# Performance work log

Hardware: AMD Instinct MI355X
Metric: run time of the kernel (lower is better)

Reference implementation:

```python
import jax, jax.numpy as jnp
import numpy as np

N, E, G, K, C = 16000, 256000, 64, 10, 32
NB, MH, NP, NE, ND, SH, RH = 8, 16, 4, 3, 6, 9, 64
R_MAX, AVG_NBR, P = 5.0, 16.0, 6
LVALS = jnp.array([0, 1, 1, 1, 2, 2, 2, 2, 2])  # l of each lm slot (l<=2)


def _silu(x):
    return x * jax.nn.sigmoid(x)


def _sph(v):
    # real spherical harmonics up to l=2 on unit vectors, e3nn 'component' normalization
    x, y, z = v[:, 0], v[:, 1], v[:, 2]
    s3, s5, s15 = 3.0 ** 0.5, 5.0 ** 0.5, 15.0 ** 0.5
    return jnp.stack([
        jnp.ones_like(x),
        s3 * x, s3 * y, s3 * z,
        s15 * x * y, s15 * y * z, 0.5 * s5 * (3.0 * z * z - 1.0),
        s15 * x * z, 0.5 * s15 * (x * x - y * y)], axis=-1)


def setup_inputs():
    key = jax.random.key(0)
    ks = jax.random.split(key, 26)

    def w(k, shape):
        fan_in = shape[-2] if len(shape) > 1 else shape[-1]
        return jax.random.normal(k, shape, jnp.float32) / np.float32(np.sqrt(fan_in))

    elems = jax.random.randint(ks[0], (N,), 0, K)
    return {
        'positions': 2.0 * jax.random.normal(ks[1], (N, 3), jnp.float32),
        'node_attrs': jax.nn.one_hot(elems, K, dtype=jnp.float32),
        'shifts': jnp.zeros((E, 3), jnp.float32),
        'E0': jax.random.normal(ks[2], (K,), jnp.float32),
        'W_embed': w(ks[3], (K, C)),
        'W_up': w(ks[4], (2, C, C)),
        'W_r1': w(ks[5], (2, NB, RH)),
        'W_r2': w(ks[6], (2, RH, RH)),
        'W_r3': w(ks[7], (2, RH, SH * C)),
        'W_sc': w(ks[8], (2, K, 3, C, C)),
        'W_prod': w(ks[9], (2, 3, C, C)),
        'Wc': w(ks[10], (2, 3, K, C, C)),
        'We1': w(ks[11], (2, C, MH)),
        'We2': w(ks[12], (2, MH, NE)),
        'Wi1': w(ks[13], (2, C, MH)),
        'Wi2': w(ks[14], (2, MH, NP)),
        'Wdp': w(ks[15], (2, C, ND)),
        'Wd1': w(ks[16], (NP, RH)),
        'bd1': jnp.zeros((RH,), jnp.float32),
        'Wd2': w(ks[17], (RH, NE)),
        'bd2': jnp.zeros((NE,), jnp.float32),
        'edge_index': jax.random.randint(ks[18], (2, E), 0, N).astype(jnp.int32),
        'batch': jnp.sort(jax.random.randint(ks[19], (N,), 0, G)).astype(jnp.int32),
    }


def _forward(edge_index, batch, positions, node_attrs, shifts, E0, W_embed, W_up,
             W_r1, W_r2, W_r3, W_sc, W_prod, Wc, We1, We2, Wi1, Wi2, Wdp,
             Wd1, bd1, Wd2, bd2):
    src, dst = edge_index[0], edge_index[1]
    vec = positions[src] - positions[dst] + shifts          # [E,3]
    r = jnp.sqrt(jnp.sum(vec * vec, axis=-1) + 1e-12)       # [E]
    sh = _sph(vec / r[:, None])                              # [E,9]
    # Bessel radial basis with polynomial cutoff envelope (p=6)
    u = r / R_MAX
    n = jnp.arange(1, NB + 1, dtype=jnp.float32)
    bess = jnp.sqrt(2.0 / R_MAX) * jnp.sin(n * jnp.pi * u[:, None]) / r[:, None]
    env = (1.0 - 0.5 * (P + 1) * (P + 2) * u ** P + P * (P + 2) * u ** (P + 1)
           - 0.5 * P * (P + 1) * u ** (P + 2))
    env = jnp.where(u < 1.0, env, 0.0)
    edge_feats = bess * env[:, None]                         # [E,NB]

    e0 = jax.ops.segment_sum(node_attrs @ E0, batch, num_segments=G)  # [G]
    feats = jnp.zeros((N, SH, C), jnp.float32).at[:, 0, :].set(node_attrs @ W_embed)

    eng_sum = jnp.zeros((G, NE), jnp.float32)
    inv_sum = jnp.zeros((G, NP), jnp.float32)
    dip_sum = jnp.zeros((G, 3, ND), jnp.float32)
    for l in range(2):
        up = feats[:, 0, :] @ W_up[l]                        # [N,C]
        Rw = _silu(edge_feats @ W_r1[l])
        Rw = _silu(Rw @ W_r2[l])
        Rw = (Rw @ W_r3[l]).reshape(E, SH, C)                # per-edge TP weights
        msg = Rw * sh[:, :, None] * up[src][:, None, :]      # [E,9,C]
        agg = jax.ops.segment_sum(msg, dst, num_segments=N) / AVG_NBR
        sc = jnp.einsum('nk,klcd,nlc->nld', node_attrs, W_sc[l][:, LVALS], feats)
        mixed = jnp.einsum('nlc,lcd->nld', agg, W_prod[l][LVALS])
        new = mixed + sc
        s0 = new[:, 0, :]
        # element-dependent symmetric-contraction on invariants (correlation 3)
        corr = (jnp.einsum('nk,kcd,nc->nd', node_attrs, Wc[l, 0], s0)
                + jnp.einsum('nk,kcd,nc->nd', node_attrs, Wc[l, 1], s0 * s0)
                + jnp.einsum('nk,kcd,nc->nd', node_attrs, Wc[l, 2], s0 * s0 * s0))
        feats = new.at[:, 0, :].add(corr)
        s = feats[:, 0, :]
        v = feats[:, 1:4, :]                                  # l=1 block [N,3,C]
        node_E = _silu(s @ We1[l]) @ We2[l]                   # [N,NE]
        node_inv = _silu(s @ Wi1[l]) @ Wi2[l]                 # [N,NP]
        node_dip = jnp.einsum('nvc,cd->nvd', v, Wdp[l])       # [N,3,ND]
        eng_sum = eng_sum + jax.ops.segment_sum(node_E, batch, num_segments=G)
        inv_sum = inv_sum + jax.ops.segment_sum(node_inv, batch, num_segments=G)
        dip_sum = dip_sum + jax.ops.segment_sum(node_dip, batch, num_segments=G)

    decoded = _silu(inv_sum @ Wd1 + bd1) @ Wd2 + bd2 + e0[:, None]   # [G,NE]
    total_e = eng_sum + e0[:, None]                                   # [G,NE]
    dip = jnp.transpose(dip_sum, (0, 2, 1))                           # [G,ND,3]
    return jnp.concatenate([decoded, total_e, dip.reshape(G, 3 * ND)], axis=-1)


def reference(positions, node_attrs, shifts, E0, W_embed, W_up, W_r1, W_r2, W_r3,
              W_sc, W_prod, Wc, We1, We2, Wi1, Wi2, Wdp, Wd1, bd1, Wd2, bd2,
              edge_index, batch):
    return _forward(edge_index, batch, positions, node_attrs, shifts, E0, W_embed,
                    W_up, W_r1, W_r2, W_r3, W_sc, W_prod, Wc, We1, We2, Wi1, Wi2,
                    Wdp, Wd1, bd1, Wd2, bd2)
```

## Files before the change

### kernel.cpp

```cpp
#include <hip/hip_runtime.h>
#include <math.h>

#define NN 16000
#define EE 256000
#define GG 64
#define KK 10
#define CC 32
#define NBB 8
#define MHH 16
#define NPP 4
#define NEE 3
#define NDD 6
#define SHH 9
#define RHH 64
#define SHCC (SHH*CC)

typedef __attribute__((ext_vector_type(8))) short s8b;
typedef __attribute__((ext_vector_type(4))) float f32x4;

__device__ __forceinline__ float siluf(float x){ return x / (1.0f + __expf(-x)); }
__device__ __forceinline__ short bf16rne(float x){
  unsigned u = __float_as_uint(x);
  unsigned r = u + 0x7FFFu + ((u>>16)&1u);
  return (short)(r>>16);
}

__global__ __launch_bounds__(256) void init_kernel(
    const float* __restrict__ attrs, const float* __restrict__ E0v,
    const float* __restrict__ Wemb, const float* __restrict__ Wup0,
    const int* __restrict__ batch,
    int* __restrict__ kidx, float* __restrict__ feats, float* __restrict__ e0g,
    float* __restrict__ up)
{
  int t = blockIdx.x*blockDim.x + threadIdx.x;
  if (t >= NN*CC) return;
  int n = t >> 5, d = t & 31;
  const float* a = attrs + n*KK;
  int k = 0; float best = a[0];
  #pragma unroll
  for (int j=1;j<KK;j++){ float v=a[j]; if (v>best){best=v;k=j;} }
  float* f = feats + n*SHCC;
  f[d] = Wemb[k*CC+d];
  #pragma unroll
  for (int s=1;s<SHH;s++) f[s*CC+d] = 0.0f;
  float accu = 0.0f;
  #pragma unroll
  for (int c=0;c<CC;c++) accu += Wemb[k*CC+c]*Wup0[c*CC+d];
  up[n*CC+d] = accu * 0.0625f;
  if (d==0){ kidx[n]=k; atomicAdd(&e0g[batch[n]], E0v[k]); }
}

__global__ __launch_bounds__(256) void hist_kernel(
    const int* __restrict__ ei, int* __restrict__ rowptr)
{
  int e = blockIdx.x*256 + threadIdx.x;
  if (e < EE) atomicAdd(&rowptr[ei[EE+e]+1], 1);
}

__global__ __launch_bounds__(1024) void scan_kernel(
    int* __restrict__ rowptr, int* __restrict__ cursor)
{
  __shared__ int part[1024];
  const int t = threadIdx.x;
  const int SEG = 16;
  const int base = t*SEG;
  int a[SEG];
  int run = 0;
  #pragma unroll
  for (int i=0;i<SEG;i++){
    int idx = base+i;
    int v = (idx <= NN) ? rowptr[idx] : 0;
    run += v; a[i] = run;
  }
  part[t] = run;
  __syncthreads();
  for (int off=1; off<1024; off<<=1){
    int v = (t>=off) ? part[t-off] : 0;
    __syncthreads();
    part[t] += v;
    __syncthreads();
  }
  int offset = (t>0) ? part[t-1] : 0;
  #pragma unroll
  for (int i=0;i<SEG;i++){
    int idx = base+i;
    if (idx <= NN){
      int val = offset + a[i];
      rowptr[idx] = val;
      if (idx < NN) cursor[idx] = val;
    }
  }
}

__global__ __launch_bounds__(256) void scatter_kernel(
    const int* __restrict__ ei, int* __restrict__ cursor, int* __restrict__ sorted)
{
  int e = blockIdx.x*256 + threadIdx.x;
  if (e < EE){
    int d = ei[EE+e];
    int p = atomicAdd(&cursor[d], 1);
    sorted[p] = e;
  }
}

__global__ __launch_bounds__(256, 2) void edge_kernel(
    const float* __restrict__ pos, const float* __restrict__ shifts,
    const float* __restrict__ Wr1, const float* __restrict__ Wr2,
    const float* __restrict__ Wr3, const float* __restrict__ up,
    const int* __restrict__ ei, const int* __restrict__ sorted,
    float* __restrict__ agg)
{
  __shared__ alignas(16) short sW3T[SHCC*RHH];
  __shared__ alignas(16) short sW2T[RHH*RHH];
  __shared__ alignas(16) float sW1T[RHH*NBB];
  __shared__ alignas(16) char  uni[64*65*4];
  __shared__ alignas(16) float sh_l[4][16*12];
  __shared__ int dst_l[64];

  for (int i=threadIdx.x; i<RHH*SHCC; i+=256){
    int kk = i/SHCC, o = i - kk*SHCC;
    sW3T[(o*RHH + kk) ^ ((o&7)<<3)] = bf16rne(Wr3[i]);
  }
  for (int i=threadIdx.x; i<RHH*RHH; i+=256){
    int k = i>>6, kk = i&63;
    sW2T[(kk*RHH + k) ^ ((kk&7)<<3)] = bf16rne(Wr2[i]);
  }
  for (int i=threadIdx.x; i<NBB*RHH; i+=256){
    int b = i>>6, k = i&63;
    sW1T[k*NBB + b] = Wr1[i];
  }
  __syncthreads();

  const int tid  = threadIdx.x;
  const int lane = tid & 63;
  const int el   = lane & 15;
  const int r    = lane >> 4;
  const int wv   = tid >> 6;
  float* msg = (float*)uni;
  float* efw = (float*)(uni + wv*512);
  short* h2w = (short*)(uni + 2048 + wv*2304);
  float* shw = sh_l[wv];
  const f32x4 zf = {0.f,0.f,0.f,0.f};
  const float PI_ = 3.14159265358979323846f;

  for (int w = blockIdx.x; w < EE/64; w += gridDim.x) {
    const int e0 = w*64 + wv*16;
    {
      const int e = sorted[e0 + el];
      const int src = ei[e], dst = ei[EE+e];
      if (r==0) dst_l[wv*16+el] = dst;
      float x = pos[src*3+0]-pos[dst*3+0]+shifts[e*3+0];
      float y = pos[src*3+1]-pos[dst*3+1]+shifts[e*3+1];
      float z = pos[src*3+2]-pos[dst*3+2]+shifts[e*3+2];
      float rr = sqrtf(x*x+y*y+z*z+1e-12f);
      float ir = 1.0f/rr;
      x*=ir; y*=ir; z*=ir;
      const float S3=1.7320508075688772f, S5h=1.1180339887498949f;
      const float S15=3.872983346207417f, S15h=1.9364916731037085f;
      if (r==0){ shw[el*12+0]=1.0f;            shw[el*12+1]=S3*x;     shw[el*12+2]=S3*y; }
      else if (r==1){ shw[el*12+3]=S3*z;       shw[el*12+4]=S15*x*y;  shw[el*12+5]=S15*y*z; }
      else if (r==2){ shw[el*12+6]=S5h*(3.0f*z*z-1.0f); shw[el*12+7]=S15*x*z; shw[el*12+8]=S15h*(x*x-y*y); }
      float u = rr*0.2f;
      float u2=u*u, u3=u2*u, u6=u3*u3;
      float env = 1.0f - 28.0f*u6 + 48.0f*u6*u - 21.0f*u6*u2;
      env = (u<1.0f)? env : 0.0f;
      env *= ir * 0.6324555320336759f;
      float n1 = (float)(r+1), n2 = (float)(r+5);
      efw[el*8 + r]     = __sinf(n1*PI_*u)*env;
      efw[el*8 + r + 4] = __sinf(n2*PI_*u)*env;
    }
    float h1v[16];
    {
      f32x4 efa = *(const f32x4*)&efw[el*8];
      f32x4 efb = *(const f32x4*)&efw[el*8+4];
      #pragma unroll
      for (int s=0;s<2;s++){
        #pragma unroll
        for (int j=0;j<8;j++){
          int kq = 32*s + 8*r + j;
          f32x4 wa = *(const f32x4*)&sW1T[kq*NBB];
          f32x4 wb = *(const f32x4*)&sW1T[kq*NBB+4];
          float acc = efa[0]*wa[0]+efa[1]*wa[1]+efa[2]*wa[2]+efa[3]*wa[3]
                    + efb[0]*wb[0]+efb[1]*wb[1]+efb[2]*wb[2]+efb[3]*wb[3];
          h1v[s*8+j] = siluf(acc);
        }
      }
    }
    s8b a1s0, a1s1;
    #pragma unroll
    for (int j=0;j<8;j++){ a1s0[j]=bf16rne(h1v[j]); a1s1[j]=bf16rne(h1v[8+j]); }

    f32x4 aw2[4];
    #pragma unroll
    for (int t=0;t<4;t++){
      int kk = 16*t + el;
      int sw = (kk&7)<<3;
      s8b b0 = *(const s8b*)&sW2T[(kk*RHH + 8*r     ) ^ sw];
      s8b b1 = *(const s8b*)&sW2T[(kk*RHH + 8*r + 32) ^ sw];
      f32x4 acc = __builtin_amdgcn_mfma_f32_16x16x32_bf16(a1s0, b0, zf, 0,0,0);
      aw2[t]    = __builtin_amdgcn_mfma_f32_16x16x32_bf16(a1s1, b1, acc, 0,0,0);
    }
    #pragma unroll
    for (int t=0;t<4;t++){
      #pragma unroll
      for (int reg=0;reg<4;reg++)
        h2w[(4*r+reg)*72 + 16*t + el] = bf16rne(siluf(aw2[t][reg]));
    }
    s8b a2s0 = *(const s8b*)&h2w[el*72 + 8*r];
    s8b a2s1 = *(const s8b*)&h2w[el*72 + 32 + 8*r];

    float upv[4][2];
    #pragma unroll
    for (int reg=0;reg<4;reg++){
      int ee = sorted[e0 + 4*r + reg];
      int s_ = ei[ee];
      upv[reg][0] = up[s_*CC + el];
      upv[reg][1] = up[s_*CC + 16 + el];
    }
    __syncthreads();

    unsigned long long runmask;
    {
      bool flag = (lane==0) || (dst_l[lane] != dst_l[lane-1]);
      runmask = __ballot(flag);
    }

    #pragma unroll
    for (int c=0;c<5;c++){
      const int tBeg = 4*c;
      const int tEnd = (c<4)? (tBeg+4) : 18;
      for (int t=tBeg;t<tEnd;t++){
        int o = 16*t + el;
        int sw = (o&7)<<3;
        s8b b0 = *(const s8b*)&sW3T[(o*RHH + 8*r     ) ^ sw];
        s8b b1 = *(const s8b*)&sW3T[(o*RHH + 8*r + 32) ^ sw];
        f32x4 acc = __builtin_amdgcn_mfma_f32_16x16x32_bf16(a2s0, b0, zf, 0,0,0);
        acc       = __builtin_amdgcn_mfma_f32_16x16x32_bf16(a2s1, b1, acc, 0,0,0);
        const int sidx = t>>1, spar = t&1;
        #pragma unroll
        for (int reg=0;reg<4;reg++){
          float v = acc[reg] * shw[(4*r+reg)*12 + sidx] * upv[reg][spar];
          msg[(wv*16 + 4*r + reg)*65 + 16*(t-tBeg) + el] = v;
        }
      }
      __syncthreads();
      {
        const int col = (c<4) ? (tid & 63) : (tid & 31);
        const bool act = (c<4) || ((tid & 63) < 32);
        const int q = tid >> 6;
        const int obase = 64*c;
        if (act){
          unsigned long long m = runmask;
          int j = 0;
          while (m){
            int s = __builtin_ctzll(m);
            m &= (m-1);
            int en = m ? __builtin_ctzll(m) : 64;
            if ((j & 3) == q){
              float a = 0.0f;
              for (int i=s;i<en;i++) a += msg[i*65 + col];
              atomicAdd(agg + (size_t)dst_l[s]*SHCC + obase + col, a);
            }
            j++;
          }
        }
      }
      __syncthreads();
    }
  }
}

__global__ __launch_bounds__(256) void node_kernel(
    const float* __restrict__ feats, float* __restrict__ fout,
    const float* __restrict__ agg,
    const int* __restrict__ kidx, const int* __restrict__ batch,
    const float* __restrict__ Wsc, const float* __restrict__ Wprod,
    const float* __restrict__ WcL,
    const float* __restrict__ We1, const float* __restrict__ We2,
    const float* __restrict__ Wi1, const float* __restrict__ Wi2,
    const float* __restrict__ Wdp, const float* __restrict__ Wup1,
    float* __restrict__ up,
    float* __restrict__ eng, float* __restrict__ inv, float* __restrict__ dip)
{
  __shared__ float s0l[8][CC];
  __shared__ float sul[8][CC];
  __shared__ float vl[8][3][CC];
  __shared__ float hl[8][CC];
  const int t = threadIdx.x;
  const int nn = t >> 5;
  const int d = t & 31;
  const int n = blockIdx.x*8 + nn;
  const int k = kidx[n];
  const int b = batch[n];
  const float* fin = feats + n*SHCC;
  const float* ag = agg + n*SHCC;
  float nw[SHH];
  const int LV[SHH] = {0,1,1,1,2,2,2,2,2};
  #pragma unroll
  for (int s=0;s<SHH;s++){
    const int lv = LV[s];
    const float* wp  = Wprod + lv*CC*CC + d;
    const float* wsc = Wsc + (k*3+lv)*CC*CC + d;
    float acc = 0.0f;
    #pragma unroll
    for (int c=0;c<CC;c++)
      acc += ag[s*CC+c]*wp[c*CC] + fin[s*CC+c]*wsc[c*CC];
    nw[s] = acc;
  }
  s0l[nn][d] = nw[0];
  vl[nn][0][d] = nw[1]; vl[nn][1][d] = nw[2]; vl[nn][2][d] = nw[3];
  __syncthreads();
  float corr = 0.0f;
  {
    const float* wc0 = WcL + (0*KK+k)*CC*CC + d;
    const float* wc1 = WcL + (1*KK+k)*CC*CC + d;
    const float* wc2 = WcL + (2*KK+k)*CC*CC + d;
    #pragma unroll
    for (int c=0;c<CC;c++){
      float s0 = s0l[nn][c];
      float s2 = s0*s0;
      corr += s0*wc0[c*CC] + s2*wc1[c*CC] + s2*s0*wc2[c*CC];
    }
  }
  float su = nw[0] + corr;
  sul[nn][d] = su;
  float* fo = fout + n*SHCC;
  fo[d] = su;
  #pragma unroll
  for (int s=1;s<SHH;s++) fo[s*CC+d] = nw[s];
  __syncthreads();
  {
    const int m = d & 15;
    const float* W = (d < MHH) ? We1 : Wi1;
    float acc = 0.0f;
    #pragma unroll
    for (int c=0;c<CC;c++) acc += sul[nn][c]*W[c*MHH+m];
    hl[nn][d] = siluf(acc);
  }
  {
    float acc = 0.0f;
    #pragma unroll
    for (int c=0;c<CC;c++) acc += sul[nn][c]*Wup1[c*CC+d];
    up[n*CC+d] = acc * 0.0625f;
  }
  __syncthreads();
  if (d < NEE){
    float acc=0.0f;
    #pragma unroll
    for (int m=0;m<MHH;m++) acc += hl[nn][m]*We2[m*NEE+d];
    atomicAdd(&eng[b*NEE+d], acc);
  } else if (d < NEE+NPP){
    const int p = d-NEE;
    float acc=0.0f;
    #pragma unroll
    for (int m=0;m<MHH;m++) acc += hl[nn][MHH+m]*Wi2[m*NPP+p];
    atomicAdd(&inv[b*NPP+p], acc);
  } else if (d < 7+3*NDD){
    const int idx = d-7;
    const int v = idx/NDD;
    const int dd = idx - v*NDD;
    float acc=0.0f;
    #pragma unroll
    for (int c=0;c<CC;c++) acc += vl[nn][v][c]*Wdp[c*NDD+dd];
    atomicAdd(&dip[(b*3+v)*NDD+dd], acc);
  }
}

__global__ __launch_bounds__(64) void final_kernel(
    const float* __restrict__ eng, const float* __restrict__ inv,
    const float* __restrict__ dip, const float* __restrict__ e0g,
    const float* __restrict__ Wd1, const float* __restrict__ bd1,
    const float* __restrict__ Wd2, const float* __restrict__ bd2,
    float* __restrict__ out)
{
  const int g = threadIdx.x;
  if (g >= GG) return;
  float e0 = e0g[g];
  float iv0=inv[g*NPP+0], iv1=inv[g*NPP+1], iv2=inv[g*NPP+2], iv3=inv[g*NPP+3];
  float o0=bd2[0], o1=bd2[1], o2=bd2[2];
  for (int m=0;m<RHH;m++){
    float hm = bd1[m] + iv0*Wd1[0*RHH+m] + iv1*Wd1[1*RHH+m] + iv2*Wd1[2*RHH+m] + iv3*Wd1[3*RHH+m];
    hm = siluf(hm);
    o0 += hm*Wd2[m*NEE+0]; o1 += hm*Wd2[m*NEE+1]; o2 += hm*Wd2[m*NEE+2];
  }
  float* og = out + g*24;
  og[0]=o0+e0; og[1]=o1+e0; og[2]=o2+e0;
  og[3]=eng[g*NEE+0]+e0; og[4]=eng[g*NEE+1]+e0; og[5]=eng[g*NEE+2]+e0;
  for (int dd=0;dd<NDD;dd++)
    for (int v=0;v<3;v++)
      og[6+dd*3+v] = dip[(g*3+v)*NDD+dd];
}

extern "C" void kernel_launch(void* const* d_in, const int* in_sizes, int n_in,
                              void* d_out, int out_size, void* d_ws, size_t ws_size,
                              hipStream_t stream)
{
  const float* pos    = (const float*)d_in[0];
  const float* attrs  = (const float*)d_in[1];
  const float* shifts = (const float*)d_in[2];
  const float* E0v    = (const float*)d_in[3];
  const float* Wemb   = (const float*)d_in[4];
  const float* Wup    = (const float*)d_in[5];
  const float* Wr1    = (const float*)d_in[6];
  const float* Wr2    = (const float*)d_in[7];
  const float* Wr3    = (const float*)d_in[8];
  const float* Wsc    = (const float*)d_in[9];
  const float* Wprod  = (const float*)d_in[10];
  const float* Wc     = (const float*)d_in[11];
  const float* We1    = (const float*)d_in[12];
  const float* We2    = (const float*)d_in[13];
  const float* Wi1    = (const float*)d_in[14];
  const float* Wi2    = (const float*)d_in[15];
  const float* Wdp    = (const float*)d_in[16];
  const float* Wd1    = (const float*)d_in[17];
  const float* bd1    = (const float*)d_in[18];
  const float* Wd2    = (const float*)d_in[19];
  const float* bd2    = (const float*)d_in[20];
  const int*   ei     = (const int*)d_in[21];
  const int*   batch  = (const int*)d_in[22];
  float* out = (float*)d_out;

  float* feats = (float*)d_ws;
  float* agg   = feats + (size_t)NN*SHCC;
  float* up    = agg   + (size_t)NN*SHCC;
  float* accum = up    + (size_t)NN*CC;
  float* e0g = accum;
  float* eng = accum + 64;
  float* inv = accum + 256;
  float* dip = accum + 512;
  int*   kidx   = (int*)(accum + 1664);
  int*   rowptr = kidx + NN;
  int*   cursor = rowptr + NN + 1;
  int*   sorted = cursor + NN;

  hipMemsetAsync(accum, 0, 1664*sizeof(float), stream);
  hipMemsetAsync(rowptr, 0, (NN+1)*sizeof(int), stream);
  init_kernel<<<(NN*CC)/256, 256, 0, stream>>>(attrs, E0v, Wemb, Wup, batch, kidx, feats, e0g, up);
  hist_kernel<<<EE/256, 256, 0, stream>>>(ei, rowptr);
  scan_kernel<<<1, 1024, 0, stream>>>(rowptr, cursor);
  scatter_kernel<<<EE/256, 256, 0, stream>>>(ei, cursor, sorted);

  for (int l=0; l<2; ++l){
    hipMemsetAsync(agg, 0, (size_t)NN*SHCC*sizeof(float), stream);
    edge_kernel<<<512, 256, 0, stream>>>(pos, shifts,
        Wr1 + l*NBB*RHH, Wr2 + l*RHH*RHH, Wr3 + l*RHH*SHCC,
        up, ei, sorted, agg);
    node_kernel<<<NN/8, 256, 0, stream>>>(feats, feats, agg, kidx, batch,
        Wsc + l*KK*3*CC*CC, Wprod + l*3*CC*CC, Wc + l*3*KK*CC*CC,
        We1 + l*CC*MHH, We2 + l*MHH*NEE, Wi1 + l*CC*MHH, Wi2 + l*MHH*NPP,
        Wdp + l*CC*NDD, Wup + 1*CC*CC, up,
        eng, inv, dip);
  }
  final_kernel<<<1, 64, 0, stream>>>(eng, inv, dip, e0g, Wd1, bd1, Wd2, bd2, out);
}
```

Before: 767.3 us.

## Group nodes by element type and stage per-element weights in shared memory

Adds a counting sort of nodes by element index, with each element's group padded to a multiple of 64. Each node_kernel block then handles 64 nodes of a single element, loading that element's self-connection and correction weights plus the shared weights into padded LDS once. Node features are staged with vectorized loads. This replaces the repeated per-thread global weight reads, at the cost of extra sort kernels, a memset, fewer blocks and heavy LDS use per block.

```diff
diff --git a/kernel.cpp b/kernel.cpp
--- a/kernel.cpp
+++ b/kernel.cpp
@@ -14,6 +14,8 @@
 #define SHH 9
 #define RHH 64
 #define SHCC (SHH*CC)
+#define NBLKN 260
+#define NPADN (NBLKN*64)
 
 typedef __attribute__((ext_vector_type(8))) short s8b;
 typedef __attribute__((ext_vector_type(4))) float f32x4;
@@ -30,7 +32,7 @@
     const float* __restrict__ Wemb, const float* __restrict__ Wup0,
     const int* __restrict__ batch,
     int* __restrict__ kidx, float* __restrict__ feats, float* __restrict__ e0g,
-    float* __restrict__ up)
+    float* __restrict__ up, int* __restrict__ khist)
 {
   int t = blockIdx.x*blockDim.x + threadIdx.x;
   if (t >= NN*CC) return;
@@ -47,7 +49,11 @@
   #pragma unroll
   for (int c=0;c<CC;c++) accu += Wemb[k*CC+c]*Wup0[c*CC+d];
   up[n*CC+d] = accu * 0.0625f;
-  if (d==0){ kidx[n]=k; atomicAdd(&e0g[batch[n]], E0v[k]); }
+  if (d==0){
+    kidx[n]=k;
+    atomicAdd(&e0g[batch[n]], E0v[k]);
+    atomicAdd(&khist[k], 1);
+  }
 }
 
 __global__ __launch_bounds__(256) void hist_kernel(
@@ -100,6 +106,27 @@
     int d = ei[EE+e];
     int p = atomicAdd(&cursor[d], 1);
     sorted[p] = e;
+  }
+}
+
+__global__ void kscan_kernel(const int* __restrict__ khist, int* __restrict__ kcursor)
+{
+  if (threadIdx.x==0 && blockIdx.x==0){
+    int off=0;
+    for (int k=0;k<KK;k++){
+      kcursor[k]=off;
+      off += ((khist[k]+63)>>6)<<6;
+    }
+  }
+}
+
+__global__ __launch_bounds__(256) void kscatter_kernel(
+    const int* __restrict__ kidx, int* __restrict__ kcursor, int* __restrict__ nsorted)
+{
+  int n = blockIdx.x*256 + threadIdx.x;
+  if (n < NN){
+    int p = atomicAdd(&kcursor[kidx[n]], 1);
+    nsorted[p] = n;
   }
 }
 
@@ -273,7 +300,8 @@
 __global__ __launch_bounds__(256) void node_kernel(
     const float* __restrict__ feats, float* __restrict__ fout,
     const float* __restrict__ agg,
-    const int* __restrict__ kidx, const int* __restrict__ batch,
+    const int* __restrict__ nsorted, const int* __restrict__ kidx,
+    const int* __restrict__ batch,
     const float* __restrict__ Wsc, const float* __restrict__ Wprod,
     const float* __restrict__ WcL,
     const float* __restrict__ We1, const float* __restrict__ We2,
@@ -282,87 +310,137 @@
     float* __restrict__ up,
     float* __restrict__ eng, float* __restrict__ inv, float* __restrict__ dip)
 {
+  __shared__ float sWp[3][32*33];
+  __shared__ float sWs[3][32*33];
+  __shared__ float sWc[3][32*33];
+  __shared__ float sWe1[32*17];
+  __shared__ float sWi1[32*17];
+  __shared__ float sWdp[32*7];
+  __shared__ float sWup[32*33];
+  __shared__ float nb[8][2][SHCC];
   __shared__ float s0l[8][CC];
   __shared__ float sul[8][CC];
   __shared__ float vl[8][3][CC];
   __shared__ float hl[8][CC];
-  const int t = threadIdx.x;
-  const int nn = t >> 5;
-  const int d = t & 31;
-  const int n = blockIdx.x*8 + nn;
-  const int k = kidx[n];
-  const int b = batch[n];
-  const float* fin = feats + n*SHCC;
-  const float* ag = agg + n*SHCC;
-  float nw[SHH];
+
+  const int base = blockIdx.x*64;
+  const int node0 = nsorted[base];
+  if (node0 < 0) return;
+  const int kb = kidx[node0];
+
+  for (int i=threadIdx.x; i<3*1024; i+=256){
+    int lv=i>>10, j=i&1023, c=j>>5, d=j&31;
+    sWp[lv][c*33+d] = Wprod[i];
+    sWs[lv][c*33+d] = Wsc[(kb*3+lv)*1024 + j];
+    sWc[lv][c*33+d] = WcL[(lv*KK+kb)*1024 + j];
+  }
+  for (int i=threadIdx.x; i<512; i+=256){
+    int c=i>>4, m=i&15;
+    sWe1[c*17+m]=We1[i]; sWi1[c*17+m]=Wi1[i];
+  }
+  for (int i=threadIdx.x; i<CC*NDD; i+=256){
+    int c=i/NDD, dd=i-c*NDD;
+    sWdp[c*7+dd]=Wdp[i];
+  }
+  for (int i=threadIdx.x; i<1024; i+=256)
+    sWup[(i>>5)*33+(i&31)] = Wup1[i];
+
+  const int t=threadIdx.x, nn=t>>5, d=t&31;
   const int LV[SHH] = {0,1,1,1,2,2,2,2,2};
-  #pragma unroll
-  for (int s=0;s<SHH;s++){
-    const int lv = LV[s];
-    const float* wp  = Wprod + lv*CC*CC + d;
-    const float* wsc = Wsc + (k*3+lv)*CC*CC + d;
-    float acc = 0.0f;
+
+  for (int p=0;p<8;p++){
+    __syncthreads();
+    const int nb0 = base + p*8;
+    for (int i=t; i<8*(SHCC/4); i+=256){
+      int ln  = i/(SHCC/4);
+      int off = (i - ln*(SHCC/4))*4;
+      int nd  = nsorted[nb0+ln];
+      float4 va, vf;
+      if (nd>=0){
+        va = *(const float4*)&agg[(size_t)nd*SHCC+off];
+        vf = *(const float4*)&feats[(size_t)nd*SHCC+off];
+      } else { va = make_float4(0,0,0,0); vf = va; }
+      *(float4*)&nb[ln][0][off] = va;
+      *(float4*)&nb[ln][1][off] = vf;
+    }
+    __syncthreads();
+    const int n = nsorted[nb0+nn];
+    const int b = (n>=0) ? batch[n] : 0;
+    float nw[SHH];
     #pragma unroll
-    for (int c=0;c<CC;c++)
-      acc += ag[s*CC+c]*wp[c*CC] + fin[s*CC+c]*wsc[c*CC];
-    nw[s] = acc;
-  }
-  s0l[nn][d] = nw[0];
-  vl[nn][0][d] = nw[1]; vl[nn][1][d] = nw[2]; vl[nn][2][d] = nw[3];
-  __syncthreads();
-  float corr = 0.0f;
-  {
-    const float* wc0 = WcL + (0*KK+k)*CC*CC + d;
-    const float* wc1 = WcL + (1*KK+k)*CC*CC + d;
-    const float* wc2 = WcL + (2*KK+k)*CC*CC + d;
-    #pragma unroll
-    for (int c=0;c<CC;c++){
-      float s0 = s0l[nn][c];
-      float s2 = s0*s0;
-      corr += s0*wc0[c*CC] + s2*wc1[c*CC] + s2*s0*wc2[c*CC];
-    }
-  }
-  float su = nw[0] + corr;
-  sul[nn][d] = su;
-  float* fo = fout + n*SHCC;
-  fo[d] = su;
-  #pragma unroll
-  for (int s=1;s<SHH;s++) fo[s*CC+d] = nw[s];
-  __syncthreads();
-  {
-    const int m = d & 15;
-    const float* W = (d < MHH) ? We1 : Wi1;
-    float acc = 0.0f;
-    #pragma unroll
-    for (int c=0;c<CC;c++) acc += sul[nn][c]*W[c*MHH+m];
-    hl[nn][d] = siluf(acc);
-  }
-  {
-    float acc = 0.0f;
-    #pragma unroll
-    for (int c=0;c<CC;c++) acc += sul[nn][c]*Wup1[c*CC+d];
-    up[n*CC+d] = acc * 0.0625f;
-  }
-  __syncthreads();
-  if (d < NEE){
-    float acc=0.0f;
-    #pragma unroll
-    for (int m=0;m<MHH;m++) acc += hl[nn][m]*We2[m*NEE+d];
-    atomicAdd(&eng[b*NEE+d], acc);
-  } else if (d < NEE+NPP){
-    const int p = d-NEE;
-    float acc=0.0f;
-    #pragma unroll
-    for (int m=0;m<MHH;m++) acc += hl[nn][MHH+m]*Wi2[m*NPP+p];
-    atomicAdd(&inv[b*NPP+p], acc);
-  } else if (d < 7+3*NDD){
-    const int idx = d-7;
-    const int v = idx/NDD;
-    const int dd = idx - v*NDD;
-    float acc=0.0f;
-    #pragma unroll
-    for (int c=0;c<CC;c++) acc += vl[nn][v][c]*Wdp[c*NDD+dd];
-    atomicAdd(&dip[(b*3+v)*NDD+dd], acc);
+    for (int s=0;s<SHH;s++){
+      const int lv = LV[s];
+      const float* xa = &nb[nn][0][s*32];
+      const float* xf = &nb[nn][1][s*32];
+      const float* wp = &sWp[lv][d];
+      const float* ws = &sWs[lv][d];
+      float acc = 0.0f;
+      #pragma unroll
+      for (int c=0;c<CC;c++)
+        acc += xa[c]*wp[c*33] + xf[c]*ws[c*33];
+      nw[s] = acc;
+    }
+    s0l[nn][d] = nw[0];
+    vl[nn][0][d] = nw[1]; vl[nn][1][d] = nw[2]; vl[nn][2][d] = nw[3];
+    __syncthreads();
+    float corr = 0.0f;
+    {
+      const float* wc0 = &sWc[0][d];
+      const float* wc1 = &sWc[1][d];
+      const float* wc2 = &sWc[2][d];
+      #pragma unroll
+      for (int c=0;c<CC;c++){
+        float s0 = s0l[nn][c];
+        float s2 = s0*s0;
+        corr += s0*wc0[c*33] + s2*wc1[c*33] + s2*s0*wc2[c*33];
+      }
+    }
+    float su = nw[0] + corr;
+    sul[nn][d] = su;
+    if (n>=0){
+      float* fo = fout + (size_t)n*SHCC;
+      fo[d] = su;
+      #pragma unroll
+      for (int s=1;s<SHH;s++) fo[s*CC+d] = nw[s];
+    }
+    __syncthreads();
+    {
+      const int m = d & 15;
+      const float* W = (d < MHH) ? sWe1 : sWi1;
+      float acc = 0.0f;
+      #pragma unroll
+      for (int c=0;c<CC;c++) acc += sul[nn][c]*W[c*17+m];
+      hl[nn][d] = siluf(acc);
+    }
+    if (n>=0){
+      float acc = 0.0f;
+      #pragma unroll
+      for (int c=0;c<CC;c++) acc += sul[nn][c]*sWup[c*33+d];
+      up[n*CC+d] = acc * 0.0625f;
+    }
+    __syncthreads();
+    if (n>=0){
+      if (d < NEE){
+        float acc=0.0f;
+        #pragma unroll
+        for (int m=0;m<MHH;m++) acc += hl[nn][m]*We2[m*NEE+d];
+        atomicAdd(&eng[b*NEE+d], acc);
+      } else if (d < NEE+NPP){
+        const int pp = d-NEE;
+        float acc=0.0f;
+        #pragma unroll
+        for (int m=0;m<MHH;m++) acc += hl[nn][MHH+m]*Wi2[m*NPP+pp];
+        atomicAdd(&inv[b*NPP+pp], acc);
+      } else if (d < 7+3*NDD){
+        const int idx = d-7;
+        const int v = idx/NDD;
+        const int dd = idx - v*NDD;
+        float acc=0.0f;
+        #pragma unroll
+        for (int c=0;c<CC;c++) acc += vl[nn][v][c]*sWdp[c*7+dd];
+        atomicAdd(&dip[(b*3+v)*NDD+dd], acc);
+      }
+    }
   }
 }
 
@@ -428,24 +506,30 @@
   float* eng = accum + 64;
   float* inv = accum + 256;
   float* dip = accum + 512;
-  int*   kidx   = (int*)(accum + 1664);
-  int*   rowptr = kidx + NN;
-  int*   cursor = rowptr + NN + 1;
-  int*   sorted = cursor + NN;
-
-  hipMemsetAsync(accum, 0, 1664*sizeof(float), stream);
+  int*   khist   = (int*)(accum + 1664);
+  int*   kcursor = khist + 16;
+  int*   kidx    = kcursor + 16;
+  int*   rowptr  = kidx + NN;
+  int*   cursor  = rowptr + NN + 1;
+  int*   sorted  = cursor + NN;
+  int*   nsorted = sorted + EE;
+
+  hipMemsetAsync(accum, 0, (1664+16)*sizeof(float), stream);
   hipMemsetAsync(rowptr, 0, (NN+1)*sizeof(int), stream);
-  init_kernel<<<(NN*CC)/256, 256, 0, stream>>>(attrs, E0v, Wemb, Wup, batch, kidx, feats, e0g, up);
+  hipMemsetAsync(nsorted, 0xFF, NPADN*sizeof(int), stream);
+  init_kernel<<<(NN*CC)/256, 256, 0, stream>>>(attrs, E0v, Wemb, Wup, batch, kidx, feats, e0g, up, khist);
   hist_kernel<<<EE/256, 256, 0, stream>>>(ei, rowptr);
   scan_kernel<<<1, 1024, 0, stream>>>(rowptr, cursor);
   scatter_kernel<<<EE/256, 256, 0, stream>>>(ei, cursor, sorted);
+  kscan_kernel<<<1, 64, 0, stream>>>(khist, kcursor);
+  kscatter_kernel<<<(NN+255)/256, 256, 0, stream>>>(kidx, kcursor, nsorted);
 
   for (int l=0; l<2; ++l){
     hipMemsetAsync(agg, 0, (size_t)NN*SHCC*sizeof(float), stream);
     edge_kernel<<<512, 256, 0, stream>>>(pos, shifts,
         Wr1 + l*NBB*RHH, Wr2 + l*RHH*RHH, Wr3 + l*RHH*SHCC,
         up, ei, sorted, agg);
-    node_kernel<<<NN/8, 256, 0, stream>>>(feats, feats, agg, kidx, batch,
+    node_kernel<<<NBLKN, 256, 0, stream>>>(feats, feats, agg, nsorted, kidx, batch,
         Wsc + l*KK*3*CC*CC, Wprod + l*3*CC*CC, Wc + l*3*KK*CC*CC,
         We1 + l*CC*MHH, We2 + l*MHH*NEE, Wi1 + l*CC*MHH, Wi2 + l*MHH*NPP,
         Wdp + l*CC*NDD, Wup + 1*CC*CC, up,
```

New measurement: 844.9 us. +10.1%, slower.
